# Optimization experiments

Hardware: AMD Instinct MI355X
Metric: run time of the kernel (lower is better)

Reference implementation:

```python
import jax, jax.numpy as jnp
import numpy as np

NC = 80        # number of classes
CONF = 0.25    # confidence threshold
RATIO = 0.1    # top-k fraction


def setup_inputs() -> dict:
    key = jax.random.key(0)
    N = 2097152
    data = jax.random.normal(key, (1, N, 4 + NC), dtype=jnp.float32)
    return {"data": data}


def reference(data):
    pred = data[0]                      # [N, 4+nc]
    cls_logits = pred[:, -NC:]          # [N, nc]
    boxes = pred[:, :4]                 # [N, 4]
    scores = jnp.max(cls_logits, axis=1)  # class_id is None -> max over classes
    n = scores.shape[0]
    k = max(1, min(n, int(np.ceil(n * float(RATIO)))))  # static k
    vals, idx = jax.lax.top_k(scores, k)   # [k], [k]
    mask = vals >= CONF                     # [k] bool
    # torch returns 0.0 when mask is empty; masked sums naturally give 0 then.
    loss = jnp.sum(jnp.where(mask, vals, 0.0))
    # output_type == 'all' -> add gathered box sums for masked top-k indices
    loss = loss + jnp.sum(jnp.where(mask[:, None], boxes[idx], 0.0))
    return loss
```

## Files before the change

kernel.cpp:

```cpp
#include <hip/hip_runtime.h>
#include <stdint.h>
#include <math.h>

#define ROWLEN 84
#define F4PR 21
#define RPB 256
#define F4PT (RPB * F4PR)
#define TIECAP 16384u

__device__ __forceinline__ uint32_t map_f(float f) {
    uint32_t u = __float_as_uint(f);
    return (u & 0x80000000u) ? ~u : (u | 0x80000000u);
}
__device__ __forceinline__ float unmap_f(uint32_t u) {
    uint32_t b = (u & 0x80000000u) ? (u & 0x7FFFFFFFu) : ~u;
    return __uint_as_float(b);
}

__device__ void find_parallel(const uint32_t* __restrict__ hist, int nbins, uint32_t target,
                              uint32_t* s, uint32_t* sc2, uint32_t* outBin, uint32_t* outAbove) {
    int tid = threadIdx.x;
    int chunks = nbins / 256;
    int base = tid * chunks;
    uint32_t part = 0;
    for (int i = 0; i < chunks; ++i) part += hist[base + i];
    s[tid] = part;
    __syncthreads();
    for (int off = 1; off < 256; off <<= 1) {
        uint32_t v = (tid + off < 256) ? s[tid + off] : 0u;
        __syncthreads();
        s[tid] += v;
        __syncthreads();
    }
    uint32_t above_next = (tid < 255) ? s[tid + 1] : 0u;
    bool mine = (s[tid] >= target) && (above_next < target);
    if (mine) { sc2[0] = (uint32_t)tid; sc2[1] = above_next; }
    __syncthreads();
    uint32_t c = sc2[0], above = sc2[1];
    if (tid == 0) {
        uint32_t acc = above;
        int b = (int)c * chunks + chunks - 1;
        for (;; --b) {
            uint32_t hb = hist[b];
            if (acc + hb >= target) break;
            acc += hb;
        }
        sc2[0] = (uint32_t)b;
        sc2[1] = acc;
    }
    __syncthreads();
    *outBin = sc2[0];
    *outAbove = sc2[1];
}

__global__ __launch_bounds__(256) void k_score_hist(const float* __restrict__ pred,
                                                    uint32_t* __restrict__ scores,
                                                    uint32_t* __restrict__ gH1,
                                                    float* __restrict__ out, int n) {
    __shared__ float pm[F4PT];
    __shared__ uint32_t h[1024];
    int tid = threadIdx.x;
    if (blockIdx.x == 0 && tid == 0) *out = 0.f;
    for (int i = tid; i < 1024; i += 256) h[i] = 0;
    uint32_t tid21 = (uint32_t)tid % 21u;
    const float4* pf4 = (const float4*)pred;
    size_t total_f4 = (size_t)n * F4PR;
    int ntiles = (n + RPB - 1) / RPB;
    for (int tile = blockIdx.x; tile < ntiles; tile += gridDim.x) {
        __syncthreads();
        size_t gbase = (size_t)tile * F4PT;
        int row0 = tile * RPB;
        if (row0 + RPB <= n) {
#pragma unroll
            for (int it = 0; it < F4PR; ++it) {
                const uint32_t BP = (21u - (4u * (uint32_t)it) % 21u) % 21u;
                float4 v = pf4[gbase + it * 256 + tid];
                float m = fmaxf(fmaxf(v.x, v.y), fmaxf(v.z, v.w));
                pm[it * 256 + tid] = (tid21 == BP) ? -INFINITY : m;
            }
        } else {
#pragma unroll
            for (int it = 0; it < F4PR; ++it) {
                const uint32_t BP = (21u - (4u * (uint32_t)it) % 21u) % 21u;
                int l = it * 256 + tid;
                size_t g = gbase + l;
                float m = -INFINITY;
                if (g < total_f4 && tid21 != BP) {
                    float4 v = pf4[g];
                    m = fmaxf(fmaxf(v.x, v.y), fmaxf(v.z, v.w));
                }
                pm[l] = m;
            }
        }
        __syncthreads();
        int row = row0 + tid;
        if (row < n) {
            const float* q = pm + tid * F4PR;
            float m = q[1];
#pragma unroll
            for (int j = 2; j <= 20; ++j) m = fmaxf(m, q[j]);
            uint32_t u = map_f(m);
            scores[row] = u;
            atomicAdd(&h[u >> 22], 1u);
        }
    }
    __syncthreads();
    for (int i = tid; i < 1024; i += 256)
        if (h[i]) atomicAdd(&gH1[i], h[i]);
}

__global__ void k_hist2f(const uint32_t* __restrict__ scores, const uint32_t* __restrict__ gH1,
                         uint32_t* __restrict__ gH2, uint32_t* __restrict__ sres,
                         int n, uint32_t K) {
    __shared__ uint32_t h[2048];
    __shared__ uint32_t s[256];
    __shared__ uint32_t sc2[2];
    for (int i = threadIdx.x; i < 2048; i += 256) h[i] = 0;
    uint32_t bin1, chi1;
    find_parallel(gH1, 1024, K, s, sc2, &bin1, &chi1);
    if (blockIdx.x == 0 && threadIdx.x == 0) { sres[0] = bin1; sres[1] = chi1; }
    int stride = gridDim.x * 256;
    for (int r = blockIdx.x * 256 + threadIdx.x; r < n; r += stride) {
        uint32_t u = scores[r];
        if ((u >> 22) == bin1) atomicAdd(&h[(u >> 11) & 0x7FFu], 1u);
    }
    __syncthreads();
    for (int i = threadIdx.x; i < 2048; i += 256)
        if (h[i]) atomicAdd(&gH2[i], h[i]);
}

__global__ void k_hist3f(const uint32_t* __restrict__ scores, const uint32_t* __restrict__ gH2,
                         uint32_t* __restrict__ gH3, uint32_t* __restrict__ sres,
                         int n, uint32_t K) {
    __shared__ uint32_t h[2048];
    __shared__ uint32_t s[256];
    __shared__ uint32_t sc2[2];
    for (int i = threadIdx.x; i < 2048; i += 256) h[i] = 0;
    uint32_t bin1 = sres[0], chi1 = sres[1];
    uint32_t bin2, chi2;
    find_parallel(gH2, 2048, K - chi1, s, sc2, &bin2, &chi2);
    if (blockIdx.x == 0 && threadIdx.x == 0) { sres[2] = bin2; sres[3] = chi2; }
    uint32_t pref = (bin1 << 11) | bin2;
    int stride = gridDim.x * 256;
    for (int r = blockIdx.x * 256 + threadIdx.x; r < n; r += stride) {
        uint32_t u = scores[r];
        if ((u >> 11) == pref) atomicAdd(&h[u & 0x7FFu], 1u);
    }
    __syncthreads();
    for (int i = threadIdx.x; i < 2048; i += 256)
        if (h[i]) atomicAdd(&gH3[i], h[i]);
}

__global__ void k_selectf(const float* __restrict__ pred, const uint32_t* __restrict__ scores,
                          const uint32_t* __restrict__ gH3, uint32_t* __restrict__ sres,
                          uint32_t* __restrict__ tieCnt, uint32_t* __restrict__ tieBuf,
                          float* __restrict__ out, int n, uint32_t K) {
    __shared__ uint32_t s[256];
    __shared__ uint32_t sc2[2];
    __shared__ float wsum[4];
    uint32_t bin1 = sres[0], chi1 = sres[1];
    uint32_t bin2 = sres[2], chi2 = sres[3];
    uint32_t bin3, chi3;
    find_parallel(gH3, 2048, K - chi1 - chi2, s, sc2, &bin3, &chi3);
    uint32_t t_u = (bin1 << 22) | (bin2 << 11) | bin3;
    uint32_t m_ties = K - (chi1 + chi2 + chi3);
    if (blockIdx.x == 0 && threadIdx.x == 0) { sres[6] = t_u; sres[7] = m_ties; }
    const uint32_t u_conf = 0xBE800000u;
    bool tcut = (t_u >= u_conf);
    float lsum = 0.f;
    int stride = gridDim.x * 256;
    for (int r = blockIdx.x * 256 + threadIdx.x; r < n; r += stride) {
        uint32_t u = scores[r];
        bool sel = tcut ? (u > t_u) : (u >= u_conf);
        if (sel) {
            float4 b = *(const float4*)(pred + (size_t)r * ROWLEN);
            lsum += unmap_f(u) + b.x + b.y + b.z + b.w;
        }
        if (tcut && u == t_u) {
            uint32_t pos = atomicAdd(tieCnt, 1u);
            if (pos < TIECAP) tieBuf[pos] = (uint32_t)r;
        }
    }
    for (int off = 32; off; off >>= 1) lsum += __shfl_down(lsum, off);
    int wid = threadIdx.x >> 6, lane = threadIdx.x & 63;
    if (lane == 0) wsum[wid] = lsum;
    __syncthreads();
    if (threadIdx.x == 0) atomicAdd(out, wsum[0] + wsum[1] + wsum[2] + wsum[3]);
}

__global__ void k_ties(const float* __restrict__ pred, const uint32_t* __restrict__ sres,
                       const uint32_t* __restrict__ tieCnt, const uint32_t* __restrict__ tieBuf,
                       float* __restrict__ out) {
    __shared__ float wsum[4];
    uint32_t t_u = sres[6];
    const uint32_t u_conf = 0xBE800000u;
    if (t_u < u_conf) return;
    uint32_t m = sres[7];
    uint32_t cnt = *tieCnt;
    if (cnt > TIECAP) cnt = TIECAP;
    float lsum = 0.f;
    if (m >= cnt) {
        for (uint32_t i = threadIdx.x; i < cnt; i += blockDim.x) {
            uint32_t r = tieBuf[i];
            float4 b = *(const float4*)(pred + (size_t)r * ROWLEN);
            lsum += b.x + b.y + b.z + b.w;
        }
    } else {
        for (uint32_t i = threadIdx.x; i < cnt; i += blockDim.x) {
            uint32_t ri = tieBuf[i];
            uint32_t rank = 0;
            for (uint32_t j = 0; j < cnt; ++j) rank += (tieBuf[j] < ri) ? 1u : 0u;
            if (rank < m) {
                float4 b = *(const float4*)(pred + (size_t)ri * ROWLEN);
                lsum += b.x + b.y + b.z + b.w;
            }
        }
    }
    for (int off = 32; off; off >>= 1) lsum += __shfl_down(lsum, off);
    int wid = threadIdx.x >> 6, lane = threadIdx.x & 63;
    if (lane == 0) wsum[wid] = lsum;
    __syncthreads();
    if (threadIdx.x == 0)
        atomicAdd(out, wsum[0] + wsum[1] + wsum[2] + wsum[3] + (float)m * unmap_f(t_u));
}

extern "C" void kernel_launch(void* const* d_in, const int* in_sizes, int n_in,
                              void* d_out, int out_size, void* d_ws, size_t ws_size,
                              hipStream_t stream) {
    const float* pred = (const float*)d_in[0];
    int n = in_sizes[0] / ROWLEN;
    double kd = ceil((double)n * 0.1);
    long kk = (long)kd;
    if (kk < 1) kk = 1;
    if (kk > n) kk = n;
    uint32_t K = (uint32_t)kk;

    uint32_t* ws32 = (uint32_t*)d_ws;
    uint32_t* scores = ws32;
    uint32_t* gH1 = ws32 + n;
    uint32_t* gH2 = gH1 + 1024;
    uint32_t* gH3 = gH2 + 2048;
    uint32_t* tieCnt = gH3 + 2048;
    uint32_t* sres = tieCnt + 16;
    uint32_t* tieBuf = sres + 16;
    float* out = (float*)d_out;

    hipMemsetAsync(gH1, 0, (1024 + 2048 + 2048 + 16) * sizeof(uint32_t), stream);

    k_score_hist<<<2048, 256, 0, stream>>>(pred, scores, gH1, out, n);
    k_hist2f<<<1024, 256, 0, stream>>>(scores, gH1, gH2, sres, n, K);
    k_hist3f<<<1024, 256, 0, stream>>>(scores, gH2, gH3, sres, n, K);
    k_selectf<<<2048, 256, 0, stream>>>(pred, scores, gH3, sres, tieCnt, tieBuf, out, n, K);
    k_ties<<<1, 256, 0, stream>>>(pred, sres, tieCnt, tieBuf, out);
}
```

Measured before the change: 201.3 us.

## Drop third radix pass; compute row max via wave shuffles; vectorize score scans

The score kernel stops staging rows through shared memory. Each wave now loads three rows' float4s and reduces the class maximum with cross-lane shuffles. The third histogram pass is removed: the select kernel collects every row whose top 21 bits match the threshold into a candidate buffer. A single-block final kernel then builds the last-level histogram from that buffer and resolves ties. Score scans use uint4 loads, which trades a full pass over the scores for atomics on a candidate buffer and more serial work in one block.

```diff
diff --git a/kernel.cpp b/kernel.cpp
--- a/kernel.cpp
+++ b/kernel.cpp
@@ -4,9 +4,7 @@
 
 #define ROWLEN 84
 #define F4PR 21
-#define RPB 256
-#define F4PT (RPB * F4PR)
-#define TIECAP 16384u
+#define CANDCAP (1u << 20)
 
 __device__ __forceinline__ uint32_t map_f(float f) {
     uint32_t u = __float_as_uint(f);
@@ -17,7 +15,7 @@
     return __uint_as_float(b);
 }
 
-__device__ void find_parallel(const uint32_t* __restrict__ hist, int nbins, uint32_t target,
+__device__ void find_parallel(const uint32_t* hist, int nbins, uint32_t target,
                               uint32_t* s, uint32_t* sc2, uint32_t* outBin, uint32_t* outAbove) {
     int tid = threadIdx.x;
     int chunks = nbins / 256;
@@ -56,52 +54,55 @@
 __global__ __launch_bounds__(256) void k_score_hist(const float* __restrict__ pred,
                                                     uint32_t* __restrict__ scores,
                                                     uint32_t* __restrict__ gH1,
+                                                    uint32_t* __restrict__ candCnt,
                                                     float* __restrict__ out, int n) {
-    __shared__ float pm[F4PT];
     __shared__ uint32_t h[1024];
     int tid = threadIdx.x;
-    if (blockIdx.x == 0 && tid == 0) *out = 0.f;
+    if (blockIdx.x == 0 && tid == 0) { *out = 0.f; *candCnt = 0u; }
     for (int i = tid; i < 1024; i += 256) h[i] = 0;
-    uint32_t tid21 = (uint32_t)tid % 21u;
+    __syncthreads();
     const float4* pf4 = (const float4*)pred;
     size_t total_f4 = (size_t)n * F4PR;
-    int ntiles = (n + RPB - 1) / RPB;
-    for (int tile = blockIdx.x; tile < ntiles; tile += gridDim.x) {
-        __syncthreads();
-        size_t gbase = (size_t)tile * F4PT;
-        int row0 = tile * RPB;
-        if (row0 + RPB <= n) {
+    int lane = tid & 63;
+    int wv = (blockIdx.x * 256 + tid) >> 6;
+    int nw = gridDim.x * 4;
+    int g = lane / 21;
+    int rel = lane - g * 21;
+    bool lv = (lane < 63);
+    int ntrip = (n + 2) / 3;
+    const int OFFS[5] = {10, 5, 3, 2, 1};
+    for (int t0 = wv * 2; t0 < ntrip; t0 += nw * 2) {
+        float mA = -INFINITY, mB = -INFINITY;
+        size_t iA = (size_t)t0 * 63 + lane;
+        size_t iB = iA + 63;
+        if (lv && rel != 0 && iA < total_f4) {
+            float4 v = pf4[iA];
+            mA = fmaxf(fmaxf(v.x, v.y), fmaxf(v.z, v.w));
+        }
+        if (lv && rel != 0 && iB < total_f4) {
+            float4 v = pf4[iB];
+            mB = fmaxf(fmaxf(v.x, v.y), fmaxf(v.z, v.w));
+        }
 #pragma unroll
-            for (int it = 0; it < F4PR; ++it) {
-                const uint32_t BP = (21u - (4u * (uint32_t)it) % 21u) % 21u;
-                float4 v = pf4[gbase + it * 256 + tid];
-                float m = fmaxf(fmaxf(v.x, v.y), fmaxf(v.z, v.w));
-                pm[it * 256 + tid] = (tid21 == BP) ? -INFINITY : m;
-            }
-        } else {
-#pragma unroll
-            for (int it = 0; it < F4PR; ++it) {
-                const uint32_t BP = (21u - (4u * (uint32_t)it) % 21u) % 21u;
-                int l = it * 256 + tid;
-                size_t g = gbase + l;
-                float m = -INFINITY;
-                if (g < total_f4 && tid21 != BP) {
-                    float4 v = pf4[g];
-                    m = fmaxf(fmaxf(v.x, v.y), fmaxf(v.z, v.w));
-                }
-                pm[l] = m;
-            }
-        }
-        __syncthreads();
-        int row = row0 + tid;
-        if (row < n) {
-            const float* q = pm + tid * F4PR;
-            float m = q[1];
-#pragma unroll
-            for (int j = 2; j <= 20; ++j) m = fmaxf(m, q[j]);
-            uint32_t u = map_f(m);
-            scores[row] = u;
-            atomicAdd(&h[u >> 22], 1u);
+        for (int k = 0; k < 5; ++k) {
+            int off = OFFS[k];
+            float oA = __shfl(mA, lane + off);
+            float oB = __shfl(mB, lane + off);
+            if (rel + off <= 20) { mA = fmaxf(mA, oA); mB = fmaxf(mB, oB); }
+        }
+        if (rel == 1) {
+            int rA = t0 * 3 + g;
+            if (rA < n) {
+                uint32_t u = map_f(mA);
+                scores[rA] = u;
+                atomicAdd(&h[u >> 22], 1u);
+            }
+            int rB = rA + 3;
+            if (rB < n) {
+                uint32_t u = map_f(mB);
+                scores[rB] = u;
+                atomicAdd(&h[u >> 22], 1u);
+            }
         }
     }
     __syncthreads();
@@ -119,8 +120,18 @@
     uint32_t bin1, chi1;
     find_parallel(gH1, 1024, K, s, sc2, &bin1, &chi1);
     if (blockIdx.x == 0 && threadIdx.x == 0) { sres[0] = bin1; sres[1] = chi1; }
+    int gid = blockIdx.x * 256 + threadIdx.x;
     int stride = gridDim.x * 256;
-    for (int r = blockIdx.x * 256 + threadIdx.x; r < n; r += stride) {
+    const uint4* s4 = (const uint4*)scores;
+    int n4 = n >> 2;
+    for (int i = gid; i < n4; i += stride) {
+        uint4 uu = s4[i];
+        if ((uu.x >> 22) == bin1) atomicAdd(&h[(uu.x >> 11) & 0x7FFu], 1u);
+        if ((uu.y >> 22) == bin1) atomicAdd(&h[(uu.y >> 11) & 0x7FFu], 1u);
+        if ((uu.z >> 22) == bin1) atomicAdd(&h[(uu.z >> 11) & 0x7FFu], 1u);
+        if ((uu.w >> 22) == bin1) atomicAdd(&h[(uu.w >> 11) & 0x7FFu], 1u);
+    }
+    for (int r = n4 * 4 + gid; r < n; r += stride) {
         uint32_t u = scores[r];
         if ((u >> 22) == bin1) atomicAdd(&h[(u >> 11) & 0x7FFu], 1u);
     }
@@ -129,56 +140,56 @@
         if (h[i]) atomicAdd(&gH2[i], h[i]);
 }
 
-__global__ void k_hist3f(const uint32_t* __restrict__ scores, const uint32_t* __restrict__ gH2,
-                         uint32_t* __restrict__ gH3, uint32_t* __restrict__ sres,
-                         int n, uint32_t K) {
-    __shared__ uint32_t h[2048];
-    __shared__ uint32_t s[256];
-    __shared__ uint32_t sc2[2];
-    for (int i = threadIdx.x; i < 2048; i += 256) h[i] = 0;
-    uint32_t bin1 = sres[0], chi1 = sres[1];
-    uint32_t bin2, chi2;
-    find_parallel(gH2, 2048, K - chi1, s, sc2, &bin2, &chi2);
-    if (blockIdx.x == 0 && threadIdx.x == 0) { sres[2] = bin2; sres[3] = chi2; }
-    uint32_t pref = (bin1 << 11) | bin2;
-    int stride = gridDim.x * 256;
-    for (int r = blockIdx.x * 256 + threadIdx.x; r < n; r += stride) {
-        uint32_t u = scores[r];
-        if ((u >> 11) == pref) atomicAdd(&h[u & 0x7FFu], 1u);
-    }
-    __syncthreads();
-    for (int i = threadIdx.x; i < 2048; i += 256)
-        if (h[i]) atomicAdd(&gH3[i], h[i]);
-}
-
-__global__ void k_selectf(const float* __restrict__ pred, const uint32_t* __restrict__ scores,
-                          const uint32_t* __restrict__ gH3, uint32_t* __restrict__ sres,
-                          uint32_t* __restrict__ tieCnt, uint32_t* __restrict__ tieBuf,
+__global__ void k_select2(const float* __restrict__ pred, const uint32_t* __restrict__ scores,
+                          const uint32_t* __restrict__ gH2, uint32_t* __restrict__ sres,
+                          uint32_t* __restrict__ candCnt, uint2* __restrict__ candBuf,
                           float* __restrict__ out, int n, uint32_t K) {
     __shared__ uint32_t s[256];
     __shared__ uint32_t sc2[2];
     __shared__ float wsum[4];
     uint32_t bin1 = sres[0], chi1 = sres[1];
-    uint32_t bin2 = sres[2], chi2 = sres[3];
-    uint32_t bin3, chi3;
-    find_parallel(gH3, 2048, K - chi1 - chi2, s, sc2, &bin3, &chi3);
-    uint32_t t_u = (bin1 << 22) | (bin2 << 11) | bin3;
-    uint32_t m_ties = K - (chi1 + chi2 + chi3);
-    if (blockIdx.x == 0 && threadIdx.x == 0) { sres[6] = t_u; sres[7] = m_ties; }
+    uint32_t bin2, chi2;
+    find_parallel(gH2, 2048, K - chi1, s, sc2, &bin2, &chi2);
+    uint32_t t21 = (bin1 << 11) | bin2;
+    uint32_t chiTot = chi1 + chi2;
+    if (blockIdx.x == 0 && threadIdx.x == 0) {
+        sres[2] = t21; sres[3] = chiTot; sres[4] = K - chiTot;
+    }
     const uint32_t u_conf = 0xBE800000u;
-    bool tcut = (t_u >= u_conf);
+    const uint32_t CONF21 = u_conf >> 11;
+    bool tcut = (t21 >= CONF21);
     float lsum = 0.f;
+    int gid = blockIdx.x * 256 + threadIdx.x;
     int stride = gridDim.x * 256;
-    for (int r = blockIdx.x * 256 + threadIdx.x; r < n; r += stride) {
+    const uint4* s4 = (const uint4*)scores;
+    int n4 = n >> 2;
+    for (int i = gid; i < n4; i += stride) {
+        uint4 uu = s4[i];
+#pragma unroll
+        for (int j = 0; j < 4; ++j) {
+            uint32_t u = (j == 0) ? uu.x : (j == 1) ? uu.y : (j == 2) ? uu.z : uu.w;
+            int r = i * 4 + j;
+            bool sel = tcut ? ((u >> 11) > t21) : (u >= u_conf);
+            if (sel) {
+                float4 b = *(const float4*)(pred + (size_t)r * ROWLEN);
+                lsum += unmap_f(u) + b.x + b.y + b.z + b.w;
+            }
+            if (tcut && (u >> 11) == t21) {
+                uint32_t pos = atomicAdd(candCnt, 1u);
+                if (pos < CANDCAP) candBuf[pos] = make_uint2((uint32_t)r, u);
+            }
+        }
+    }
+    for (int r = n4 * 4 + gid; r < n; r += stride) {
         uint32_t u = scores[r];
-        bool sel = tcut ? (u > t_u) : (u >= u_conf);
+        bool sel = tcut ? ((u >> 11) > t21) : (u >= u_conf);
         if (sel) {
             float4 b = *(const float4*)(pred + (size_t)r * ROWLEN);
             lsum += unmap_f(u) + b.x + b.y + b.z + b.w;
         }
-        if (tcut && u == t_u) {
-            uint32_t pos = atomicAdd(tieCnt, 1u);
-            if (pos < TIECAP) tieBuf[pos] = (uint32_t)r;
+        if (tcut && (u >> 11) == t21) {
+            uint32_t pos = atomicAdd(candCnt, 1u);
+            if (pos < CANDCAP) candBuf[pos] = make_uint2((uint32_t)r, u);
         }
     }
     for (int off = 32; off; off >>= 1) lsum += __shfl_down(lsum, off);
@@ -188,40 +199,69 @@
     if (threadIdx.x == 0) atomicAdd(out, wsum[0] + wsum[1] + wsum[2] + wsum[3]);
 }
 
-__global__ void k_ties(const float* __restrict__ pred, const uint32_t* __restrict__ sres,
-                       const uint32_t* __restrict__ tieCnt, const uint32_t* __restrict__ tieBuf,
-                       float* __restrict__ out) {
+__global__ void k_final(const float* __restrict__ pred, const uint32_t* __restrict__ sres,
+                        const uint32_t* __restrict__ candCnt, const uint2* __restrict__ candBuf,
+                        float* __restrict__ out) {
+    __shared__ uint32_t h[2048];
+    __shared__ uint32_t s[256];
+    __shared__ uint32_t sc2[2];
     __shared__ float wsum[4];
-    uint32_t t_u = sres[6];
+    __shared__ uint32_t tb[1024];
+    __shared__ uint32_t tc;
+    uint32_t t21 = sres[2];
     const uint32_t u_conf = 0xBE800000u;
-    if (t_u < u_conf) return;
-    uint32_t m = sres[7];
-    uint32_t cnt = *tieCnt;
-    if (cnt > TIECAP) cnt = TIECAP;
+    const uint32_t CONF21 = u_conf >> 11;
+    if (t21 < CONF21) return;
+    uint32_t mprime = sres[4];
+    uint32_t cc = *candCnt;
+    if (cc > CANDCAP) cc = CANDCAP;
+    int tid = threadIdx.x;
+    for (int i = tid; i < 2048; i += 256) h[i] = 0;
+    if (tid == 0) tc = 0;
+    __syncthreads();
+    for (uint32_t i = tid; i < cc; i += 256) atomicAdd(&h[candBuf[i].y & 0x7FFu], 1u);
+    __syncthreads();
+    uint32_t bin3, chi3;
+    find_parallel(h, 2048, mprime, s, sc2, &bin3, &chi3);
+    uint32_t t_u = (t21 << 11) | bin3;
+    uint32_t mt = mprime - chi3;
     float lsum = 0.f;
-    if (m >= cnt) {
-        for (uint32_t i = threadIdx.x; i < cnt; i += blockDim.x) {
-            uint32_t r = tieBuf[i];
-            float4 b = *(const float4*)(pred + (size_t)r * ROWLEN);
+    for (uint32_t i = tid; i < cc; i += 256) {
+        uint2 c = candBuf[i];
+        uint32_t low = c.y & 0x7FFu;
+        if (low > bin3) {
+            float4 b = *(const float4*)(pred + (size_t)c.x * ROWLEN);
+            lsum += unmap_f(c.y) + b.x + b.y + b.z + b.w;
+        } else if (low == bin3) {
+            uint32_t p = atomicAdd(&tc, 1u);
+            if (p < 1024) tb[p] = c.x;
+        }
+    }
+    __syncthreads();
+    uint32_t tcnt = tc;
+    if (tcnt > 1024) tcnt = 1024;
+    if (mt >= tcnt) {
+        for (uint32_t i = tid; i < tcnt; i += 256) {
+            float4 b = *(const float4*)(pred + (size_t)tb[i] * ROWLEN);
             lsum += b.x + b.y + b.z + b.w;
         }
     } else {
-        for (uint32_t i = threadIdx.x; i < cnt; i += blockDim.x) {
-            uint32_t ri = tieBuf[i];
+        for (uint32_t i = tid; i < tcnt; i += 256) {
+            uint32_t ri = tb[i];
             uint32_t rank = 0;
-            for (uint32_t j = 0; j < cnt; ++j) rank += (tieBuf[j] < ri) ? 1u : 0u;
-            if (rank < m) {
+            for (uint32_t j = 0; j < tcnt; ++j) rank += (tb[j] < ri) ? 1u : 0u;
+            if (rank < mt) {
                 float4 b = *(const float4*)(pred + (size_t)ri * ROWLEN);
                 lsum += b.x + b.y + b.z + b.w;
             }
         }
     }
     for (int off = 32; off; off >>= 1) lsum += __shfl_down(lsum, off);
-    int wid = threadIdx.x >> 6, lane = threadIdx.x & 63;
+    int wid = tid >> 6, lane = tid & 63;
     if (lane == 0) wsum[wid] = lsum;
     __syncthreads();
-    if (threadIdx.x == 0)
-        atomicAdd(out, wsum[0] + wsum[1] + wsum[2] + wsum[3] + (float)m * unmap_f(t_u));
+    if (tid == 0)
+        atomicAdd(out, wsum[0] + wsum[1] + wsum[2] + wsum[3] + (float)mt * unmap_f(t_u));
 }
 
 extern "C" void kernel_launch(void* const* d_in, const int* in_sizes, int n_in,
@@ -239,17 +279,15 @@
     uint32_t* scores = ws32;
     uint32_t* gH1 = ws32 + n;
     uint32_t* gH2 = gH1 + 1024;
-    uint32_t* gH3 = gH2 + 2048;
-    uint32_t* tieCnt = gH3 + 2048;
-    uint32_t* sres = tieCnt + 16;
-    uint32_t* tieBuf = sres + 16;
+    uint32_t* candCnt = gH2 + 2048;
+    uint32_t* sres = candCnt + 16;
+    uint2* candBuf = (uint2*)(sres + 16);
     float* out = (float*)d_out;
 
-    hipMemsetAsync(gH1, 0, (1024 + 2048 + 2048 + 16) * sizeof(uint32_t), stream);
-
-    k_score_hist<<<2048, 256, 0, stream>>>(pred, scores, gH1, out, n);
+    hipMemsetAsync(gH1, 0, (1024 + 2048) * sizeof(uint32_t), stream);
+
+    k_score_hist<<<2048, 256, 0, stream>>>(pred, scores, gH1, candCnt, out, n);
     k_hist2f<<<1024, 256, 0, stream>>>(scores, gH1, gH2, sres, n, K);
-    k_hist3f<<<1024, 256, 0, stream>>>(scores, gH2, gH3, sres, n, K);
-    k_selectf<<<2048, 256, 0, stream>>>(pred, scores, gH3, sres, tieCnt, tieBuf, out, n, K);
-    k_ties<<<1, 256, 0, stream>>>(pred, sres, tieCnt, tieBuf, out);
-}
+    k_select2<<<2048, 256, 0, stream>>>(pred, scores, gH2, sres, candCnt, candBuf, out, n, K);
+    k_final<<<1, 256, 0, stream>>>(pred, sres, candCnt, candBuf, out);
+}
```

After: 209.4 us. 4.0% more time.
